# Kernel optimization log

Hardware: AMD Instinct MI355X
Metric: run time of the kernel (lower is better)

The kernel has to match this reference:

```python
import jax, jax.numpy as jnp
import numpy as np

WAY, NQ, C, H = 5, 150, 640, 10
TEMP, TEMP_ATTN = 0.2, 5.0


def _conv2d(x, w):
    return jax.lax.conv_general_dilated(x, w, (1, 1), ((0, 0), (0, 0)),
                                        dimension_numbers=('NCHW', 'OIHW', 'NCHW'))


def _conv3d(x, w, pad):
    return jax.lax.conv_general_dilated(x, w, (1, 1, 1), pad,
                                        dimension_numbers=('NCDHW', 'OIDHW', 'NCDHW'))


def _affine(x, g, b):
    # eval-mode BatchNorm folded to per-channel affine
    sh = (1, -1) + (1,) * (x.ndim - 2)
    return x * g.reshape(sh) + b.reshape(sh)


def _gnorm(x, axis, eps=1e-5):
    m = jnp.mean(x, axis=axis, keepdims=True)
    v = jnp.var(x, axis=axis, ddof=1, keepdims=True)  # torch.var is unbiased
    return (x - m) / jnp.sqrt(v + eps)


def _sep_conv4d(x, w2, g2, b2, w1, g1, b1, wp, gp, bp):
    # RENet SepConv4d: 3x3 conv over (Hs,Ws), relu, 3x3 conv over (Hq,Wq), 1x1 channel proj
    B, c, u, v, h, w = x.shape
    y = x.reshape(B, c, u, v, h * w)
    y = _conv3d(y, w2, ((1, 1), (1, 1), (0, 0)))  # kernel (3,3,1) over (u,v)
    y = jax.nn.relu(_affine(y, g2, b2))
    y = y.reshape(B, c, u * v, h, w)
    y = _conv3d(y, w1, ((0, 0), (1, 1), (1, 1)))  # kernel (1,3,3) over (h,w)
    y = _affine(y, g1, b1)
    y = _conv2d(y.reshape(B, c, u * v * h, w), wp)  # 1x1 projection to out channels
    y = _affine(y, gp, bp)
    return y.reshape(B, wp.shape[0], u, v, h, w)


def setup_inputs() -> dict:
    key = jax.random.key(0)
    ks = jax.random.split(key, 10)
    d = {}
    d['spt'] = jax.random.normal(ks[0], (1, WAY, C, H, H), jnp.float32)
    d['qry'] = jax.random.normal(ks[1], (NQ, C, H, H), jnp.float32)
    d['cca1x1_w'] = jax.random.normal(ks[2], (64, C, 1, 1), jnp.float32) * 0.05
    d['cca1x1_g'] = jnp.ones((64,), jnp.float32)
    d['cca1x1_b'] = jnp.zeros((64,), jnp.float32)
    # SepConv4d layer 0: 1 -> 16 channels
    d['s0_w2'] = jax.random.normal(ks[3], (1, 1, 3, 3, 1), jnp.float32) * 0.3
    d['s0_g2'] = jnp.ones((1,), jnp.float32); d['s0_b2'] = jnp.zeros((1,), jnp.float32)
    d['s0_w1'] = jax.random.normal(ks[4], (1, 1, 1, 3, 3), jnp.float32) * 0.3
    d['s0_g1'] = jnp.ones((1,), jnp.float32); d['s0_b1'] = jnp.zeros((1,), jnp.float32)
    d['s0_wp'] = jax.random.normal(ks[5], (16, 1, 1, 1), jnp.float32) * 0.3
    d['s0_gp'] = jnp.ones((16,), jnp.float32); d['s0_bp'] = jnp.zeros((16,), jnp.float32)
    # SepConv4d layer 1: 16 -> 1 channels
    d['s1_w2'] = jax.random.normal(ks[6], (16, 16, 3, 3, 1), jnp.float32) * 0.1
    d['s1_g2'] = jnp.ones((16,), jnp.float32); d['s1_b2'] = jnp.zeros((16,), jnp.float32)
    d['s1_w1'] = jax.random.normal(ks[7], (16, 16, 1, 3, 3), jnp.float32) * 0.1
    d['s1_g1'] = jnp.ones((16,), jnp.float32); d['s1_b1'] = jnp.zeros((16,), jnp.float32)
    d['s1_wp'] = jax.random.normal(ks[8], (1, 16, 1, 1), jnp.float32) * 0.3
    d['s1_gp'] = jnp.ones((1,), jnp.float32); d['s1_bp'] = jnp.zeros((1,), jnp.float32)
    return d


def reference(spt, qry, cca1x1_w, cca1x1_g, cca1x1_b,
              s0_w2, s0_g2, s0_b2, s0_w1, s0_g1, s0_b1, s0_wp, s0_gp, s0_bp,
              s1_w2, s1_g2, s1_b2, s1_w1, s1_g1, s1_b1, s1_wp, s1_gp, s1_bp):
    spt = spt[0]                                             # [way, C, H, W]
    spt = spt - jnp.mean(spt, axis=1, keepdims=True)         # normalize_feature
    qry = qry - jnp.mean(qry, axis=1, keepdims=True)

    def feat(x):
        y = jax.nn.relu(_affine(_conv2d(x, cca1x1_w), cca1x1_g, cca1x1_b))
        n = jnp.sqrt(jnp.sum(y * y, axis=1, keepdims=True))
        return y / jnp.maximum(n, 1e-8)                      # F.normalize(p=2, dim=1)

    s, q = feat(spt), feat(qry)                              # [way,64,H,W], [nq,64,H,W]
    corr = jnp.einsum('wcij,qckl->qwijkl', s, q)             # [nq,way,Hs,Ws,Hq,Wq]
    nq, way, Hs, Ws, Hq, Wq = corr.shape

    x = corr.reshape(nq * way, 1, Hs, Ws, Hq, Wq)
    x = _sep_conv4d(x, s0_w2, s0_g2, s0_b2, s0_w1, s0_g1, s0_b1, s0_wp, s0_gp, s0_bp)
    x = jax.nn.relu(x)
    x = _sep_conv4d(x, s1_w2, s1_g2, s1_b2, s1_w1, s1_g1, s1_b1, s1_wp, s1_gp, s1_bp)

    cs = _gnorm(x.reshape(nq, way, Hs * Ws, Hq, Wq), 2)
    cq = _gnorm(x.reshape(nq, way, Hs, Ws, Hq * Wq), 4)
    a_s = jax.nn.softmax(cs / TEMP_ATTN, axis=2).reshape(nq, way, Hs, Ws, Hq, Wq).sum(axis=(4, 5))
    a_q = jax.nn.softmax(cq / TEMP_ATTN, axis=4).reshape(nq, way, Hs, Ws, Hq, Wq).sum(axis=(2, 3))

    sp = (a_s[:, :, None] * spt[None]).mean(axis=(-1, -2))   # [nq,way,C]
    qp = (a_q[:, :, None] * qry[:, None]).mean(axis=(-1, -2))
    num = jnp.sum(sp * qp, axis=-1)
    den = jnp.maximum(jnp.linalg.norm(sp, axis=-1), 1e-8) * jnp.maximum(jnp.linalg.norm(qp, axis=-1), 1e-8)
    return (num / den) / TEMP                                # [nq, way]
```

## Files before the change

kernel.cpp:

```cpp
#include <hip/hip_runtime.h>
#include <cstdint>
#include <cstddef>

#define NQT   150
#define WAYT  5
#define CCH   640

typedef _Float16 f16;
typedef _Float16 f16x2 __attribute__((ext_vector_type(2)));
typedef _Float16 f16x4 __attribute__((ext_vector_type(4)));
typedef _Float16 f16x8 __attribute__((ext_vector_type(8)));
typedef float    f32x4 __attribute__((ext_vector_type(4)));

static __device__ __forceinline__ f16x2 pkrtz(float a, float b){
  return __builtin_bit_cast(f16x2, __builtin_amdgcn_cvt_pkrtz(a, b));
}

#define CP_A     0
#define CP_B     16
#define CP_G2    32
#define CP_B2    48
#define CP_W20   64
#define CP_W10   73
#define CP_SC    82
#define CP_T9    96
#define GS_STRIDE 1076

static __device__ __forceinline__ float stencil9(int k, int n, const float* __restrict__ w9){
  if (k >= 100 || n >= 100) return 0.f;
  const int a = n/10, b = n%10, a2 = k/10, b2 = k%10;
  const int dA = a2 - a + 1, dB = b2 - b + 1;
  if ((unsigned)dA > 2u || (unsigned)dB > 2u) return 0.f;
  return w9[dA*3 + dB];
}

__global__ __launch_bounds__(256) void k_prep_all(
    const float* __restrict__ W,
    const float* __restrict__ s0_w2, const float* __restrict__ s0_g2, const float* __restrict__ s0_b2,
    const float* __restrict__ s0_w1, const float* __restrict__ s0_g1, const float* __restrict__ s0_b1,
    const float* __restrict__ s0_wp, const float* __restrict__ s0_gp, const float* __restrict__ s0_bp,
    const float* __restrict__ s1_w2, const float* __restrict__ s1_g2, const float* __restrict__ s1_b2,
    const float* __restrict__ s1_w1, const float* __restrict__ s1_g1, const float* __restrict__ s1_b1,
    const float* __restrict__ s1_wp, const float* __restrict__ s1_gp, const float* __restrict__ s1_bp,
    float* __restrict__ cp, f16* __restrict__ Apack, f16* __restrict__ Wf2,
    f16* __restrict__ MuF, f16* __restrict__ MhF,
    f16* __restrict__ W65, float* __restrict__ wsum)
{
  const int b = blockIdx.x, t = threadIdx.x;
  if (b == 0){
    for (int e = t; e < 2560; e += 256){
      int p = e / 512, r = e % 512, l = r / 8, j = r % 8;
      int kb = l >> 4;
      int tap = 2*p + (kb >> 1);
      int cin = (kb & 1)*8 + j;
      int co = l & 15;
      float v = 0.f;
      if (tap <= 8){
        int du = tap / 3, dv = tap % 3;
        v = s1_w2[((co*16 + cin)*3 + du)*3 + dv];
      }
      Apack[e] = (f16)v;
    }
    const float gp1 = s1_gp[0];
    {
      int l = t >> 2, j = t & 3;
      int tap = l & 15, ci = ((l >> 4) << 2) + j;
      float v = 0.f;
      if (tap <= 8){
        for (int co = 0; co < 16; co++)
          v += gp1 * s1_wp[co] * s1_g1[co] * s1_w1[(co*16 + ci)*9 + tap];
      }
      Wf2[t] = (f16)v;
    }
    if (t < 144){
      int tap = t / 16, co = t % 16;
      float s = 0.f;
      for (int cin = 0; cin < 16; cin++){
        float wv = (float)(f16)s1_w2[((co*16 + cin)*3 + tap/3)*3 + tap%3];
        float rb = fmaxf((float)(f16)s0_bp[cin], 0.f);
        s += wv * rb;
      }
      cp[CP_T9 + t] = s;
    }
    if (t < 16){
      cp[CP_A + t]  = s0_gp[t] * s0_wp[t];
      cp[CP_B + t]  = s0_bp[t];
      cp[CP_G2 + t] = s1_g2[t];
      cp[CP_B2 + t] = s1_b2[t];
    }
    if (t < 9){ cp[CP_W20 + t] = s0_w2[t]; cp[CP_W10 + t] = s0_w1[t]; }
    if (t == 0){
      cp[CP_SC + 0] = s0_g2[0]; cp[CP_SC + 1] = s0_b2[0];
      cp[CP_SC + 2] = s0_g1[0]; cp[CP_SC + 3] = s0_b1[0];
      float kk = 0.f;
      for (int co = 0; co < 16; co++) kk += s1_wp[co] * s1_b1[co];
      cp[CP_SC + 4] = gp1 * kk + s1_bp[0];
    }
  } else if (b <= 14){
    const bool isMu = (b <= 7);
    f16* dst = isMu ? MuF : MhF;
    const float* w9 = isMu ? s0_w2 : s0_w1;
    const int base = (isMu ? (b-1) : (b-8)) * 2048;
    #pragma unroll
    for (int e2 = 0; e2 < 8; e2++){
      const int idx = base + e2*256 + t;
      const int j = idx & 7, l2 = (idx >> 3) & 63, ktnt = idx >> 9;
      const int kt = ktnt & 3, nt = ktnt >> 2;
      const int n = nt*16 + (l2 & 15);
      const int k = kt*32 + ((l2 >> 4) & 3)*8 + j;
      dst[idx] = (f16)stencil9(k, n, w9);
    }
  } else if (b <= 39){
    const int base = (b - 15) * 2048;
    #pragma unroll
    for (int e2 = 0; e2 < 8; e2++){
      const int idx = base + e2*256 + t;
      const int row = idx / 640, c = idx - row*640;
      float v = 0.f;
      if (row < 64) v = W[row*640 + c];
      else if (row == 64) v = 1.f;
      W65[idx] = (f16)v;
    }
  } else {
    const int o = t >> 2, qq = t & 3;
    float s = 0.f;
    for (int c = qq; c < 640; c += 4) s += W[o*640 + c];
    s += __shfl_xor(s, 1); s += __shfl_xor(s, 2);
    if (qq == 0) wsum[o] = s;
  }
}

__device__ __forceinline__ void feat_stage4(const float* __restrict__ x, int pixoff, int kt,
                                            f16* __restrict__ dst, int t){
  if (t < 224){
    const int cc = t / 7, qd = t % 7;
    float4 v4 = make_float4(0.f, 0.f, 0.f, 0.f);
    if (pixoff + qd*4 + 4 <= 100)
      v4 = *(const float4*)(x + (size_t)(kt*32 + cc)*100 + pixoff + qd*4);
    dst[(qd*4+0)*40 + cc] = (f16)v4.x;
    dst[(qd*4+1)*40 + cc] = (f16)v4.y;
    dst[(qd*4+2)*40 + cc] = (f16)v4.z;
    dst[(qd*4+3)*40 + cc] = (f16)v4.w;
  }
}

__global__ __launch_bounds__(256) void k_feat(
    const float* __restrict__ spt, const float* __restrict__ qry,
    const f16* __restrict__ W65, const float* __restrict__ wsum,
    const float* __restrict__ gg, const float* __restrict__ bb,
    f16* __restrict__ s16, f16* __restrict__ q16,
    float* __restrict__ sptm, float* __restrict__ qrym)
{
  __shared__ f16 Xs[2][32*40];
  __shared__ float Ys[32*85];
  __shared__ float sg[64], sb[64], sw[64];
  const int b = blockIdx.x;
  const int n = b >> 2, quarter = b & 3;
  const int pixbase = quarter * 28;
  const float* x; f16* out16; float* mout;
  if (n < 5){ x = spt + (size_t)n*64000; out16 = s16 + (size_t)n*7168; mout = sptm + n*100; }
  else { x = qry + (size_t)(n-5)*64000; out16 = q16 + (size_t)(n-5)*7168; mout = qrym + (size_t)(n-5)*100; }
  const int t = threadIdx.x, l = t & 63, wid = t >> 6;
  const int r16 = l & 15, kbq = (l >> 4) & 3;

  if (t < 40){
    const f16x8 z8 = {(f16)0,(f16)0,(f16)0,(f16)0,(f16)0,(f16)0,(f16)0,(f16)0};
    const int bu = t / 20, rr = (t % 20) / 5, o = t % 5;
    *(f16x8*)(Xs[bu] + (28 + rr)*40 + o*8) = z8;
  }
  if (t >= 64 && t < 128){ sg[t-64] = gg[t-64]; sb[t-64] = bb[t-64]; sw[t-64] = wsum[t-64]; }

  int mts[3], nts[3];
  #pragma unroll
  for (int s = 0; s < 3; s++){ const int mn = wid + s*4; mts[s] = mn >> 1; nts[s] = mn & 1; }
  f32x4 acc[3];
  #pragma unroll
  for (int s = 0; s < 3; s++) acc[s] = (f32x4){0.f,0.f,0.f,0.f};

  feat_stage4(x, pixbase, 0, Xs[0], t);
  __syncthreads();
  for (int kt = 0; kt < 20; kt++){
    if (kt < 19) feat_stage4(x, pixbase, kt+1, Xs[(kt+1)&1], t);
    const f16* xb = Xs[kt&1];
    #pragma unroll
    for (int s = 0; s < 3; s++){
      const int mn = wid + s*4;
      if (mn < 10){
        const f16x8 a8 = *(const f16x8*)(W65 + (size_t)(mts[s]*16 + r16)*640 + kt*32 + kbq*8);
        const f16x8 b8 = *(const f16x8*)(xb + (nts[s]*16 + r16)*40 + kbq*8);
        acc[s] = __builtin_amdgcn_mfma_f32_16x16x32_f16(a8, b8, acc[s], 0, 0, 0);
      }
    }
    __syncthreads();
  }
  #pragma unroll
  for (int s = 0; s < 3; s++){
    const int mn = wid + s*4;
    if (mn < 10){
      const int col = nts[s]*16 + r16, rb = mts[s]*16 + kbq*4;
      #pragma unroll
      for (int r = 0; r < 4; r++) Ys[col*85 + rb + r] = acc[s][r];
    }
  }
  __syncthreads();

  if (t < 224){
    const int pixl = t >> 3, oo = t & 7;
    const int pixg = pixbase + pixl;
    const bool ok = (pixg < 100);
    const float m = Ys[pixl*85 + 64] * (1.f/640.f);
    float yr[8]; float ssq = 0.f;
    #pragma unroll
    for (int j = 0; j < 8; j++){
      const int o = oo*8 + j;
      float yv = 0.f;
      if (ok) yv = fmaxf(sg[o]*(Ys[pixl*85 + o] - sw[o]*m) + sb[o], 0.f);
      yr[j] = yv; ssq += yv*yv;
    }
    ssq += __shfl_xor(ssq, 1); ssq += __shfl_xor(ssq, 2); ssq += __shfl_xor(ssq, 4);
    const float inv = ok ? (1.f / fmaxf(sqrtf(ssq), 1e-8f)) : 0.f;
    #pragma unroll
    for (int j2 = 0; j2 < 4; j2++){
      f16x2 hv = { (f16)(yr[2*j2]*inv), (f16)(yr[2*j2+1]*inv) };
      *(f16x2*)(out16 + (size_t)pixg*64 + oo*8 + 2*j2) = hv;
    }
    if (oo == 0 && ok) mout[pixg] = m;
  }
}

__global__ __launch_bounds__(256) void k_z(
    const f16* __restrict__ s16, const f16* __restrict__ q16,
    const float* __restrict__ cp, const f16* __restrict__ MuF, const f16* __restrict__ MhF,
    f16* __restrict__ z)
{
  __shared__ __align__(16) f16 smz[112*120 + 112*120 + 16];
  f16* cbT = smz;
  f16* tS  = smz + 112*120;
  const int pair = blockIdx.x;
  const int q = pair / WAYT, w = pair % WAYT;
  const int t = threadIdx.x, l = t & 63, wid = t >> 6;
  const int r16 = l & 15, kb = (l >> 4) & 3;

  {
    const f16x8 z8 = {(f16)0,(f16)0,(f16)0,(f16)0,(f16)0,(f16)0,(f16)0,(f16)0};
    if (t < 112){
      *(f16x8*)(cbT + t*120 + 112) = z8;
      *(f16x8*)(tS  + t*120 + 112) = z8;
    }
    if (t < 16) tS[112*120 + t] = (f16)0;
    if (t >= 240 && t < 248) tS[t - 240] = (f16)0;
  }

  const f16* sbase = s16 + (size_t)w * 7168;
  const f16* qbase = q16 + (size_t)q * 7168;

  for (int mn = wid; mn < 49; mn += 4){
    const int mt = mn / 7, nt = mn - (mn/7)*7;
    const f16x8 a0 = *(const f16x8*)(sbase + (mt*16 + r16)*64 + kb*8);
    const f16x8 a1 = *(const f16x8*)(sbase + (mt*16 + r16)*64 + 32 + kb*8);
    const f16x8 b0 = *(const f16x8*)(qbase + (nt*16 + r16)*64 + kb*8);
    const f16x8 b1 = *(const f16x8*)(qbase + (nt*16 + r16)*64 + 32 + kb*8);
    f32x4 acc = {0.f,0.f,0.f,0.f};
    acc = __builtin_amdgcn_mfma_f32_16x16x32_f16(a0, b0, acc, 0, 0, 0);
    acc = __builtin_amdgcn_mfma_f32_16x16x32_f16(a1, b1, acc, 0, 0, 0);
    union { f16x4 v4; f16x2 h2[2]; } hv;
    hv.h2[0] = pkrtz(acc[0], acc[1]);
    hv.h2[1] = pkrtz(acc[2], acc[3]);
    *(f16x4*)(cbT + (nt*16 + r16)*120 + mt*16 + kb*4) = hv.v4;
  }
  __syncthreads();

  const float g20 = cp[CP_SC+0], b20 = cp[CP_SC+1];
  for (int mn = wid; mn < 49; mn += 4){
    const int mt = mn / 7, nt = mn - (mn/7)*7;
    f32x4 acc = {0.f,0.f,0.f,0.f};
    #pragma unroll
    for (int kt = 0; kt < 4; kt++){
      const f16x8 a8 = *(const f16x8*)(cbT + (mt*16 + r16)*120 + kt*32 + kb*8);
      const f16x8 b8 = *(const f16x8*)(MuF + (size_t)(nt*4 + kt)*512 + l*8);
      acc = __builtin_amdgcn_mfma_f32_16x16x32_f16(a8, b8, acc, 0, 0, 0);
    }
    union { f16x4 v4; f16x2 h2[2]; } hv;
    hv.h2[0] = pkrtz(fmaxf(g20*acc[0] + b20, 0.f), fmaxf(g20*acc[1] + b20, 0.f));
    hv.h2[1] = pkrtz(fmaxf(g20*acc[2] + b20, 0.f), fmaxf(g20*acc[3] + b20, 0.f));
    *(f16x4*)(tS + (nt*16 + r16)*120 + mt*16 + kb*4) = hv.v4;
  }
  __syncthreads();

  const float g10 = cp[CP_SC+2], b10 = cp[CP_SC+3];
  for (int mn = wid; mn < 49; mn += 4){
    const int mt = mn / 7, nt = mn - (mn/7)*7;
    f32x4 acc = {0.f,0.f,0.f,0.f};
    #pragma unroll
    for (int kt = 0; kt < 4; kt++){
      const f16x8 a8 = *(const f16x8*)(tS + (mt*16 + r16)*120 + kt*32 + kb*8);
      const f16x8 b8 = *(const f16x8*)(MhF + (size_t)(nt*4 + kt)*512 + l*8);
      acc = __builtin_amdgcn_mfma_f32_16x16x32_f16(a8, b8, acc, 0, 0, 0);
    }
    const int hw = nt*16 + r16;
    if (hw < 100){
      #pragma unroll
      for (int r = 0; r < 4; r++){
        const int uv = mt*16 + kb*4 + r;
        if (uv < 100) z[(size_t)pair*10000 + uv*100 + hw] = (f16)(g10*acc[r] + b10);
      }
    }
  }
}

__global__ __launch_bounds__(256, 6) void k_l1(
    const f16* __restrict__ z, const float* __restrict__ cp,
    const f16* __restrict__ Apack, const f16* __restrict__ Wf2, f16* __restrict__ F)
{
  __shared__ f16 z3[3*1216];
  __shared__ f16 Gs[9*GS_STRIDE];
  const int u = blockIdx.x, pair = blockIdx.y;
  const int t = threadIdx.x, l = t & 63, wid = t >> 6;
  const int r16 = l & 15, kb = (l >> 4) & 3;
  const int khi = kb & 1, half = kb >> 1;

  for (int e = t; e < 1824; e += 256){
    const int du = e / 608, c2 = e - du*608;
    const int ur = u + du - 1;
    const int colb = c2*2;
    const int g = colb - 100;
    f16x2 v = {(f16)0, (f16)0};
    if (ur >= 0 && ur <= 9 && g >= 0 && g < 1000)
      v = *(const f16x2*)(z + (size_t)pair*10000 + ur*1000 + g);
    *(f16x2*)(z3 + du*1216 + colb) = v;
  }

  f16x2 Ac2[4], Bc2[4];
  {
    const float4 a4a = ((const float4*)(cp + CP_A))[khi*2];
    const float4 a4b = ((const float4*)(cp + CP_A))[khi*2+1];
    const float4 b4a = ((const float4*)(cp + CP_B))[khi*2];
    const float4 b4b = ((const float4*)(cp + CP_B))[khi*2+1];
    Ac2[0] = (f16x2){(f16)a4a.x,(f16)a4a.y}; Ac2[1] = (f16x2){(f16)a4a.z,(f16)a4a.w};
    Ac2[2] = (f16x2){(f16)a4b.x,(f16)a4b.y}; Ac2[3] = (f16x2){(f16)a4b.z,(f16)a4b.w};
    Bc2[0] = (f16x2){(f16)b4a.x,(f16)b4a.y}; Bc2[1] = (f16x2){(f16)b4a.z,(f16)b4a.w};
    Bc2[2] = (f16x2){(f16)b4b.x,(f16)b4b.y}; Bc2[3] = (f16x2){(f16)b4b.z,(f16)b4b.w};
  }
  f16x8 af[5];
  #pragma unroll
  for (int p = 0; p < 5; p++) af[p] = ((const f16x8*)Apack)[p*64 + l];
  const f16x4 wf = ((const f16x4*)Wf2)[l];

  float gv[4], bm[4], bv0[4], bv9[4];
  #pragma unroll
  for (int r = 0; r < 4; r++){
    const int co = kb*4 + r;
    gv[r] = cp[CP_G2 + co];
    const float b0 = cp[CP_B2 + co];
    float c0 = 0.f, cv0 = 0.f, cv9 = 0.f;
    #pragma unroll
    for (int du = 0; du < 3; du++){
      const int ur = u + du - 1;
      const float t0 = cp[CP_T9 + (du*3+0)*16 + co];
      const float t1 = cp[CP_T9 + (du*3+1)*16 + co];
      const float t2 = cp[CP_T9 + (du*3+2)*16 + co];
      if (ur < 0 || ur > 9) c0 += t0 + t1 + t2;
      else { cv0 += t0; cv9 += t2; }
    }
    bm[r]  = b0 - gv[r]*c0;
    bv0[r] = bm[r] - gv[r]*cv0;
    bv9[r] = bm[r] - gv[r]*cv9;
  }
  int zoffE[5];
  #pragma unroll
  for (int p = 0; p < 5; p++){
    const int tap = 2*p + half;
    const int du = (tap <= 8) ? tap/3 : 0;
    const int dv = (tap <= 8) ? tap%3 : 0;
    zoffE[p] = du*1216 + dv*100;
  }
  __syncthreads();

  const f16x2 zero2 = {(f16)0, (f16)0};
  #pragma unroll 1
  for (int i = 0; i < 16; i++){
    const int cbase = wid*256 + i*16;
    if (cbase >= 1008) break;
    const int c = cbase + r16;
    const int v = (c * 5243) >> 19;
    f32x4 acc = {0.f,0.f,0.f,0.f};
    #pragma unroll
    for (int p = 0; p < 5; p++){
      const f16 zv = z3[zoffE[p] + c];
      const f16x2 zz = {zv, zv};
      union { f16x8 v8; f16x2 h2[4]; } bu;
      #pragma unroll
      for (int j2 = 0; j2 < 4; j2++){
        f16x2 r2 = Ac2[j2] * zz + Bc2[j2];
        bu.h2[j2] = __builtin_elementwise_max(r2, zero2);
      }
      acc = __builtin_amdgcn_mfma_f32_16x16x32_f16(af[p], bu.v8, acc, 0, 0, 0);
    }
    const bool isv0 = (v == 0), isv9 = (v == 9);
    float rr[4];
    #pragma unroll
    for (int r = 0; r < 4; r++){
      const float bsel = isv0 ? bv0[r] : (isv9 ? bv9[r] : bm[r]);
      rr[r] = fmaxf(fmaf(gv[r], acc[r], bsel), 0.f);
    }
    union { f16x4 v4; f16x2 h2[2]; } t1u;
    t1u.h2[0] = pkrtz(rr[0], rr[1]);
    t1u.h2[1] = pkrtz(rr[2], rr[3]);
    f32x4 g = {0.f,0.f,0.f,0.f};
    g = __builtin_amdgcn_mfma_f32_16x16x16f16(wf, t1u.v4, g, 0, 0, 0);
    #pragma unroll
    for (int r = 0; r < 4; r++){
      const int tap = kb*4 + r;
      if (tap <= 8) Gs[tap*GS_STRIDE + 16 + c] = (f16)g[r];
    }
  }
  __syncthreads();

  const float Kc = cp[CP_SC+4];
  #pragma unroll 1
  for (int oo = 0; oo < 4; oo++){
    const int c = t + oo*256;
    if (c < 1000){
      const int hw = c - ((c * 5243) >> 19) * 100;
      const int h = (hw * 205) >> 11, w2 = hw - h*10;
      float o = Kc;
      #pragma unroll
      for (int dh = 0; dh < 3; dh++){
        #pragma unroll
        for (int dw = 0; dw < 3; dw++){
          const bool okg = ((unsigned)(h + dh - 1) <= 9u) && ((unsigned)(w2 + dw - 1) <= 9u);
          const float gvv = (float)Gs[(dh*3+dw)*GS_STRIDE + 16 + c + (dh-1)*10 + (dw-1)];
          o += okg ? gvv : 0.f;
        }
      }
      F[(size_t)pair*10000 + u*1000 + c] = (f16)o;
    }
  }
}

__global__ __launch_bounds__(256) void k_attn_a(const f16* __restrict__ F, float* __restrict__ asq)
{
  __shared__ float fb[100*101 + 4];
  __shared__ float isc[100], ccs[100], isr[100], ccr[100];
  const int pair = blockIdx.x;
  const int t = threadIdx.x;
  const float L2T = 1.4426950408889634f * 0.2f;

  for (int e = t; e < 10000; e += 256)
    fb[(e/100)*101 + (e%100)] = (float)F[(size_t)pair*10000 + e];
  __syncthreads();

  {
    const int line = t & 127;
    const bool isCol = t < 128;
    if (line < 100){
      const int base = isCol ? line : line*101;
      const int stride = isCol ? 101 : 1;
      float s = 0.f, ss = 0.f;
      for (int i = 0; i < 100; i++){ const float x = fb[base + i*stride]; s += x; ss += x*x; }
      const float m = s * 0.01f;
      const float var = (ss - 100.f*m*m) * (1.f/99.f);
      const float is2 = rsqrtf(var + 1e-5f) * L2T;
      float S = 0.f;
      for (int i = 0; i < 100; i++) S += exp2f((fb[base + i*stride] - m) * is2);
      const float cc = m*is2 + log2f(S);
      if (isCol){ isc[line] = is2; ccs[line] = cc; }
      else      { isr[line] = is2; ccr[line] = cc; }
    }
  }
  __syncthreads();
  {
    const int line = t & 127;
    if (line < 100){
      if (t < 128){
        float a = 0.f;
        for (int k = 0; k < 100; k++)
          a += exp2f(fb[line*101 + k] * isc[k] - ccs[k]);
        asq[(size_t)pair*256 + line] = a;
      } else {
        float a = 0.f;
        for (int k = 0; k < 100; k++)
          a += exp2f(fb[k*101 + line] * isr[k] - ccr[k]);
        asq[(size_t)pair*256 + 128 + line] = a;
      }
    } else {
      asq[(size_t)pair*256 + t] = 0.f;
    }
  }
}

__global__ __launch_bounds__(256) void k_spqp(
    const float* __restrict__ spt, const float* __restrict__ qry,
    const float* __restrict__ asq, float* __restrict__ P)
{
  const int b = blockIdx.x;
  const int t = threadIdx.x, l = t & 63, wid = t >> 6;
  const int r16 = l & 15, kb = (l >> 4) & 3;

  if (b < 50){
    const int w = b / 10, c0 = (b % 10) * 64;
    const int c = c0 + wid*16 + r16;
    f16x8 bf[4];
    #pragma unroll
    for (int kt = 0; kt < 4; kt++){
      const int kbase = kt*32 + kb*8;
      float v[8];
      #pragma unroll
      for (int j = 0; j < 8; j++){
        const int k = kbase + j;
        v[j] = (k < 100) ? spt[(size_t)w*64000 + (size_t)c*100 + k] : 0.f;
      }
      union { f16x8 v8; f16x2 h2[4]; } u;
      #pragma unroll
      for (int j2 = 0; j2 < 4; j2++) u.h2[j2] = pkrtz(v[2*j2], v[2*j2+1]);
      bf[kt] = u.v8;
    }
    #pragma unroll 1
    for (int mt = 0; mt < 10; mt++){
      const int qr = mt*16 + r16;
      f32x4 acc = {0.f,0.f,0.f,0.f};
      #pragma unroll
      for (int kt = 0; kt < 4; kt++){
        const int kbase = kt*32 + kb*8;
        float v[8];
        #pragma unroll
        for (int j = 0; j < 8; j++)
          v[j] = (qr < 150) ? asq[(size_t)(qr*5 + w)*256 + kbase + j] : 0.f;
        union { f16x8 v8; f16x2 h2[4]; } u;
        #pragma unroll
        for (int j2 = 0; j2 < 4; j2++) u.h2[j2] = pkrtz(v[2*j2], v[2*j2+1]);
        acc = __builtin_amdgcn_mfma_f32_16x16x32_f16(u.v8, bf[kt], acc, 0, 0, 0);
      }
      #pragma unroll
      for (int r = 0; r < 4; r++){
        const int q2 = mt*16 + kb*4 + r;
        if (q2 < 150) P[(size_t)(q2*5 + w)*1280 + c0 + wid*16 + (l & 15)] = acc[r];
      }
    }
  } else {
    const int idx = b - 50, q = idx >> 1, chalf = idx & 1;
    f16x8 af[4];
    #pragma unroll
    for (int kt = 0; kt < 4; kt++){
      const int kbase = kt*32 + kb*8;
      float v[8];
      #pragma unroll
      for (int j = 0; j < 8; j++)
        v[j] = (r16 < 5) ? asq[(size_t)(q*5 + r16)*256 + 128 + kbase + j] : 0.f;
      union { f16x8 v8; f16x2 h2[4]; } u;
      #pragma unroll
      for (int j2 = 0; j2 < 4; j2++) u.h2[j2] = pkrtz(v[2*j2], v[2*j2+1]);
      af[kt] = u.v8;
    }
    #pragma unroll 1
    for (int nt = chalf*20 + wid; nt < chalf*20 + 20; nt += 4){
      const int c = nt*16 + r16;
      f32x4 acc = {0.f,0.f,0.f,0.f};
      #pragma unroll
      for (int kt = 0; kt < 4; kt++){
        const int kbase = kt*32 + kb*8;
        float v[8];
        #pragma unroll
        for (int j = 0; j < 8; j++){
          const int k = kbase + j;
          v[j] = (k < 100) ? qry[(size_t)q*64000 + (size_t)c*100 + k] : 0.f;
        }
        union { f16x8 v8; f16x2 h2[4]; } u;
        #pragma unroll
        for (int j2 = 0; j2 < 4; j2++) u.h2[j2] = pkrtz(v[2*j2], v[2*j2+1]);
        acc = __builtin_amdgcn_mfma_f32_16x16x32_f16(af[kt], u.v8, acc, 0, 0, 0);
      }
      #pragma unroll
      for (int r = 0; r < 4; r++){
        const int w2 = kb*4 + r;
        if (w2 < 5) P[(size_t)(q*5 + w2)*1280 + 640 + nt*16 + (l & 15)] = acc[r];
      }
    }
  }
}

__global__ __launch_bounds__(256) void k_cos(
    const float* __restrict__ P, const float* __restrict__ asq,
    const float* __restrict__ sptm, const float* __restrict__ qrym,
    float* __restrict__ out)
{
  __shared__ float pred[4];
  __shared__ float MsMq[2];
  __shared__ float red[12];
  const int pair = blockIdx.x;
  const int q = pair / WAYT, w = pair % WAYT;
  const int t = threadIdx.x, wid = t >> 6;

  float pm = 0.f;
  if (t < 100) pm = asq[(size_t)pair*256 + t] * sptm[w*100 + t];
  else if (t >= 128 && t < 228) pm = asq[(size_t)pair*256 + t] * qrym[q*100 + (t - 128)];
  #pragma unroll
  for (int m = 1; m < 64; m <<= 1) pm += __shfl_xor(pm, m);
  if ((t & 63) == 0) pred[wid] = pm;
  __syncthreads();
  if (t == 0) MsMq[0] = pred[0] + pred[1];
  if (t == 1) MsMq[1] = pred[2] + pred[3];
  __syncthreads();
  const float Ms = MsMq[0], Mq = MsMq[1];

  float d0 = 0.f, d1 = 0.f, d2 = 0.f;
  for (int c = t; c < 640; c += 256){
    const float sp = P[(size_t)pair*1280 + c] - Ms;
    const float qp = P[(size_t)pair*1280 + 640 + c] - Mq;
    d0 += sp*qp; d1 += sp*sp; d2 += qp*qp;
  }
  #pragma unroll
  for (int m = 1; m < 64; m <<= 1){
    d0 += __shfl_xor(d0, m); d1 += __shfl_xor(d1, m); d2 += __shfl_xor(d2, m);
  }
  if ((t & 63) == 0){ red[wid*3+0] = d0; red[wid*3+1] = d1; red[wid*3+2] = d2; }
  __syncthreads();
  if (t == 0){
    float e0 = 0.f, e1 = 0.f, e2 = 0.f;
    #pragma unroll
    for (int k = 0; k < 4; k++){ e0 += red[k*3]; e1 += red[k*3+1]; e2 += red[k*3+2]; }
    const float den = fmaxf(sqrtf(e1), 1e-8f) * fmaxf(sqrtf(e2), 1e-8f);
    out[pair] = (e0 / den) * 5.0f;
  }
}

extern "C" void kernel_launch(void* const* d_in, const int* in_sizes, int n_in,
                              void* d_out, int out_size, void* d_ws, size_t ws_size,
                              hipStream_t stream)
{
  (void)in_sizes; (void)n_in; (void)out_size; (void)ws_size;
  const float* spt = (const float*)d_in[0];
  const float* qry = (const float*)d_in[1];
  const float* Wc  = (const float*)d_in[2];
  const float* gc  = (const float*)d_in[3];
  const float* bc  = (const float*)d_in[4];

  float* ws    = (float*)d_ws;
  float* cp    = ws;
  float* wsum  = ws + 256;
  float* sptm  = ws + 320;
  float* qrym  = ws + 820;
  f16*  Apack  = (f16*)(ws + 15872);
  f16*  Wf2    = (f16*)(ws + 17152);
  f16*  W65    = (f16*)(ws + 17280);
  f16*  MuF    = (f16*)(ws + 42880);
  f16*  MhF    = (f16*)(ws + 50048);
  f16*  s16    = (f16*)(ws + 57216);
  f16*  q16    = (f16*)(ws + 75136);
  f16*  z      = (f16*)(ws + 612736);
  f16*  F      = (f16*)(ws + 4362736);
  float* asq   = ws + 75136;
  float* P     = ws + 612736;

  k_prep_all<<<41, 256, 0, stream>>>(
      Wc,
      (const float*)d_in[5],  (const float*)d_in[6],  (const float*)d_in[7],
      (const float*)d_in[8],  (const float*)d_in[9],  (const float*)d_in[10],
      (const float*)d_in[11], (const float*)d_in[12], (const float*)d_in[13],
      (const float*)d_in[14], (const float*)d_in[15], (const float*)d_in[16],
      (const float*)d_in[17], (const float*)d_in[18], (const float*)d_in[19],
      (const float*)d_in[20], (const float*)d_in[21], (const float*)d_in[22],
      cp, Apack, Wf2, MuF, MhF, W65, wsum);
  k_feat<<<620, 256, 0, stream>>>(spt, qry, W65, wsum, gc, bc, s16, q16, sptm, qrym);
  k_z<<<NQT*WAYT, 256, 0, stream>>>(s16, q16, cp, MuF, MhF, z);
  {
    dim3 grid(10, NQT*WAYT);
    k_l1<<<grid, 256, 0, stream>>>(z, cp, Apack, Wf2, F);
  }
  k_attn_a<<<NQT*WAYT, 256, 0, stream>>>(F, asq);
  k_spqp<<<350, 256, 0, stream>>>(spt, qry, asq, P);
  k_cos<<<NQT*WAYT, 256, 0, stream>>>(P, asq, sptm, qrym, (float*)d_out);
}
```

Before: 252.5 us.

## Widen k_l1 to 512 threads, split tap 8 into 16x16x16 MFMA, prepack fp16 operands

k_l1 now launches 512 threads per block with eight waves. The padded ninth tap, previously handled by a fifth 16x16x32 MFMA, is now done with a smaller 16x16x16 MFMA using new prepacked Wf8 weights, and register arrays shrink. Separately, the support features are converted to fp16 in the prep kernel, and k_attn_a writes an fp16 copy of the attention sums. k_spqp then loads its MFMA operands as vectors instead of doing scalar fp32 loads and packing them. The workspace layout shifts to hold the new buffers, and the prep kernel gains 200 blocks.

```diff
diff --git a/kernel.cpp b/kernel.cpp
--- a/kernel.cpp
+++ b/kernel.cpp
@@ -35,16 +35,16 @@
 }
 
 __global__ __launch_bounds__(256) void k_prep_all(
-    const float* __restrict__ W,
+    const float* __restrict__ spt, const float* __restrict__ W,
     const float* __restrict__ s0_w2, const float* __restrict__ s0_g2, const float* __restrict__ s0_b2,
     const float* __restrict__ s0_w1, const float* __restrict__ s0_g1, const float* __restrict__ s0_b1,
     const float* __restrict__ s0_wp, const float* __restrict__ s0_gp, const float* __restrict__ s0_bp,
     const float* __restrict__ s1_w2, const float* __restrict__ s1_g2, const float* __restrict__ s1_b2,
     const float* __restrict__ s1_w1, const float* __restrict__ s1_g1, const float* __restrict__ s1_b1,
     const float* __restrict__ s1_wp, const float* __restrict__ s1_gp, const float* __restrict__ s1_bp,
-    float* __restrict__ cp, f16* __restrict__ Apack, f16* __restrict__ Wf2,
+    float* __restrict__ cp, f16* __restrict__ Apack, f16* __restrict__ Wf2, f16* __restrict__ Wf8,
     f16* __restrict__ MuF, f16* __restrict__ MhF,
-    f16* __restrict__ W65, float* __restrict__ wsum)
+    f16* __restrict__ W65, float* __restrict__ wsum, f16* __restrict__ spt16)
 {
   const int b = blockIdx.x, t = threadIdx.x;
   if (b == 0){
@@ -72,6 +72,11 @@
       }
       Wf2[t] = (f16)v;
     }
+    {
+      int l = t >> 2, j = t & 3;
+      int co = l & 15, cin = ((l >> 4) << 2) + j;
+      Wf8[t] = (f16)s1_w2[((co*16 + cin)*3 + 2)*3 + 2];
+    }
     if (t < 144){
       int tap = t / 16, co = t % 16;
       float s = 0.f;
@@ -121,12 +126,21 @@
       else if (row == 64) v = 1.f;
       W65[idx] = (f16)v;
     }
-  } else {
+  } else if (b == 40){
     const int o = t >> 2, qq = t & 3;
     float s = 0.f;
     for (int c = qq; c < 640; c += 4) s += W[o*640 + c];
     s += __shfl_xor(s, 1); s += __shfl_xor(s, 2);
     if (qq == 0) wsum[o] = s;
+  } else {
+    const int base = (b - 41) * 2048;
+    #pragma unroll
+    for (int e2 = 0; e2 < 8; e2++){
+      const int idx = base + e2*256 + t;
+      const int w = idx / 81920, r = idx % 81920;
+      const int c = r >> 7, k = r & 127;
+      spt16[idx] = (k < 100) ? (f16)spt[(size_t)w*64000 + c*100 + k] : (f16)0;
+    }
   }
 }
 
@@ -308,9 +322,10 @@
   }
 }
 
-__global__ __launch_bounds__(256, 6) void k_l1(
+__global__ __launch_bounds__(512, 8) void k_l1(
     const f16* __restrict__ z, const float* __restrict__ cp,
-    const f16* __restrict__ Apack, const f16* __restrict__ Wf2, f16* __restrict__ F)
+    const f16* __restrict__ Apack, const f16* __restrict__ Wf2, const f16* __restrict__ Wf8,
+    f16* __restrict__ F)
 {
   __shared__ f16 z3[3*1216];
   __shared__ f16 Gs[9*GS_STRIDE];
@@ -319,7 +334,7 @@
   const int r16 = l & 15, kb = (l >> 4) & 3;
   const int khi = kb & 1, half = kb >> 1;
 
-  for (int e = t; e < 1824; e += 256){
+  for (int e = t; e < 1824; e += 512){
     const int du = e / 608, c2 = e - du*608;
     const int ur = u + du - 1;
     const int colb = c2*2;
@@ -341,10 +356,18 @@
     Bc2[0] = (f16x2){(f16)b4a.x,(f16)b4a.y}; Bc2[1] = (f16x2){(f16)b4a.z,(f16)b4a.w};
     Bc2[2] = (f16x2){(f16)b4b.x,(f16)b4b.y}; Bc2[3] = (f16x2){(f16)b4b.z,(f16)b4b.w};
   }
-  f16x8 af[5];
-  #pragma unroll
-  for (int p = 0; p < 5; p++) af[p] = ((const f16x8*)Apack)[p*64 + l];
-  const f16x4 wf = ((const f16x4*)Wf2)[l];
+  f16x2 Ac8[2], Bc8[2];
+  {
+    const float4 a4 = ((const float4*)(cp + CP_A))[kb];
+    const float4 b4 = ((const float4*)(cp + CP_B))[kb];
+    Ac8[0] = (f16x2){(f16)a4.x,(f16)a4.y}; Ac8[1] = (f16x2){(f16)a4.z,(f16)a4.w};
+    Bc8[0] = (f16x2){(f16)b4.x,(f16)b4.y}; Bc8[1] = (f16x2){(f16)b4.z,(f16)b4.w};
+  }
+  f16x8 af[4];
+  #pragma unroll
+  for (int p = 0; p < 4; p++) af[p] = ((const f16x8*)Apack)[p*64 + l];
+  const f16x4 wf  = ((const f16x4*)Wf2)[l];
+  const f16x4 wf8 = ((const f16x4*)Wf8)[l];
 
   float gv[4], bm[4], bv0[4], bv9[4];
   #pragma unroll
@@ -366,26 +389,26 @@
     bv0[r] = bm[r] - gv[r]*cv0;
     bv9[r] = bm[r] - gv[r]*cv9;
   }
-  int zoffE[5];
-  #pragma unroll
-  for (int p = 0; p < 5; p++){
+  int zoffE[4];
+  #pragma unroll
+  for (int p = 0; p < 4; p++){
     const int tap = 2*p + half;
-    const int du = (tap <= 8) ? tap/3 : 0;
-    const int dv = (tap <= 8) ? tap%3 : 0;
+    const int du = tap/3, dv = tap%3;
     zoffE[p] = du*1216 + dv*100;
   }
+  const int zoff8 = 2*1216 + 2*100;
   __syncthreads();
 
   const f16x2 zero2 = {(f16)0, (f16)0};
   #pragma unroll 1
-  for (int i = 0; i < 16; i++){
-    const int cbase = wid*256 + i*16;
+  for (int i = 0; i < 8; i++){
+    const int cbase = (wid + i*8)*16;
     if (cbase >= 1008) break;
     const int c = cbase + r16;
     const int v = (c * 5243) >> 19;
     f32x4 acc = {0.f,0.f,0.f,0.f};
     #pragma unroll
-    for (int p = 0; p < 5; p++){
+    for (int p = 0; p < 4; p++){
       const f16 zv = z3[zoffE[p] + c];
       const f16x2 zz = {zv, zv};
       union { f16x8 v8; f16x2 h2[4]; } bu;
@@ -395,6 +418,14 @@
         bu.h2[j2] = __builtin_elementwise_max(r2, zero2);
       }
       acc = __builtin_amdgcn_mfma_f32_16x16x32_f16(af[p], bu.v8, acc, 0, 0, 0);
+    }
+    {
+      const f16 zv8 = z3[zoff8 + c];
+      const f16x2 z8 = {zv8, zv8};
+      union { f16x4 v4; f16x2 h2[2]; } b8u;
+      b8u.h2[0] = __builtin_elementwise_max(Ac8[0]*z8 + Bc8[0], zero2);
+      b8u.h2[1] = __builtin_elementwise_max(Ac8[1]*z8 + Bc8[1], zero2);
+      acc = __builtin_amdgcn_mfma_f32_16x16x16f16(wf8, b8u.v4, acc, 0, 0, 0);
     }
     const bool isv0 = (v == 0), isv9 = (v == 9);
     float rr[4];
@@ -418,8 +449,8 @@
 
   const float Kc = cp[CP_SC+4];
   #pragma unroll 1
-  for (int oo = 0; oo < 4; oo++){
-    const int c = t + oo*256;
+  for (int oo = 0; oo < 2; oo++){
+    const int c = t + oo*512;
     if (c < 1000){
       const int hw = c - ((c * 5243) >> 19) * 100;
       const int h = (hw * 205) >> 11, w2 = hw - h*10;
@@ -438,7 +469,8 @@
   }
 }
 
-__global__ __launch_bounds__(256) void k_attn_a(const f16* __restrict__ F, float* __restrict__ asq)
+__global__ __launch_bounds__(256) void k_attn_a(const f16* __restrict__ F,
+                                                float* __restrict__ asq, f16* __restrict__ asqh)
 {
   __shared__ float fb[100*101 + 4];
   __shared__ float isc[100], ccs[100], isr[100], ccr[100];
@@ -477,21 +509,24 @@
         for (int k = 0; k < 100; k++)
           a += exp2f(fb[line*101 + k] * isc[k] - ccs[k]);
         asq[(size_t)pair*256 + line] = a;
+        asqh[(size_t)pair*256 + line] = (f16)a;
       } else {
         float a = 0.f;
         for (int k = 0; k < 100; k++)
           a += exp2f(fb[k*101 + line] * isr[k] - ccr[k]);
         asq[(size_t)pair*256 + 128 + line] = a;
+        asqh[(size_t)pair*256 + 128 + line] = (f16)a;
       }
     } else {
       asq[(size_t)pair*256 + t] = 0.f;
+      asqh[(size_t)pair*256 + t] = (f16)0;
     }
   }
 }
 
 __global__ __launch_bounds__(256) void k_spqp(
-    const float* __restrict__ spt, const float* __restrict__ qry,
-    const float* __restrict__ asq, float* __restrict__ P)
+    const f16* __restrict__ spt16, const float* __restrict__ qry,
+    const f16* __restrict__ asqh, float* __restrict__ P)
 {
   const int b = blockIdx.x;
   const int t = threadIdx.x, l = t & 63, wid = t >> 6;
@@ -502,34 +537,16 @@
     const int c = c0 + wid*16 + r16;
     f16x8 bf[4];
     #pragma unroll
-    for (int kt = 0; kt < 4; kt++){
-      const int kbase = kt*32 + kb*8;
-      float v[8];
-      #pragma unroll
-      for (int j = 0; j < 8; j++){
-        const int k = kbase + j;
-        v[j] = (k < 100) ? spt[(size_t)w*64000 + (size_t)c*100 + k] : 0.f;
-      }
-      union { f16x8 v8; f16x2 h2[4]; } u;
-      #pragma unroll
-      for (int j2 = 0; j2 < 4; j2++) u.h2[j2] = pkrtz(v[2*j2], v[2*j2+1]);
-      bf[kt] = u.v8;
-    }
+    for (int kt = 0; kt < 4; kt++)
+      bf[kt] = *(const f16x8*)(spt16 + ((size_t)w*640 + c)*128 + kt*32 + kb*8);
     #pragma unroll 1
     for (int mt = 0; mt < 10; mt++){
       const int qr = mt*16 + r16;
       f32x4 acc = {0.f,0.f,0.f,0.f};
       #pragma unroll
       for (int kt = 0; kt < 4; kt++){
-        const int kbase = kt*32 + kb*8;
-        float v[8];
-        #pragma unroll
-        for (int j = 0; j < 8; j++)
-          v[j] = (qr < 150) ? asq[(size_t)(qr*5 + w)*256 + kbase + j] : 0.f;
-        union { f16x8 v8; f16x2 h2[4]; } u;
-        #pragma unroll
-        for (int j2 = 0; j2 < 4; j2++) u.h2[j2] = pkrtz(v[2*j2], v[2*j2+1]);
-        acc = __builtin_amdgcn_mfma_f32_16x16x32_f16(u.v8, bf[kt], acc, 0, 0, 0);
+        const f16x8 au = *(const f16x8*)(asqh + (size_t)(qr*5 + w)*256 + kt*32 + kb*8);
+        acc = __builtin_amdgcn_mfma_f32_16x16x32_f16(au, bf[kt], acc, 0, 0, 0);
       }
       #pragma unroll
       for (int r = 0; r < 4; r++){
@@ -539,19 +556,10 @@
     }
   } else {
     const int idx = b - 50, q = idx >> 1, chalf = idx & 1;
-    f16x8 af[4];
-    #pragma unroll
-    for (int kt = 0; kt < 4; kt++){
-      const int kbase = kt*32 + kb*8;
-      float v[8];
-      #pragma unroll
-      for (int j = 0; j < 8; j++)
-        v[j] = (r16 < 5) ? asq[(size_t)(q*5 + r16)*256 + 128 + kbase + j] : 0.f;
-      union { f16x8 v8; f16x2 h2[4]; } u;
-      #pragma unroll
-      for (int j2 = 0; j2 < 4; j2++) u.h2[j2] = pkrtz(v[2*j2], v[2*j2+1]);
-      af[kt] = u.v8;
-    }
+    f16x8 af4[4];
+    #pragma unroll
+    for (int kt = 0; kt < 4; kt++)
+      af4[kt] = *(const f16x8*)(asqh + (size_t)(q*5 + r16)*256 + 128 + kt*32 + kb*8);
     #pragma unroll 1
     for (int nt = chalf*20 + wid; nt < chalf*20 + 20; nt += 4){
       const int c = nt*16 + r16;
@@ -565,10 +573,10 @@
           const int k = kbase + j;
           v[j] = (k < 100) ? qry[(size_t)q*64000 + (size_t)c*100 + k] : 0.f;
         }
-        union { f16x8 v8; f16x2 h2[4]; } u;
+        union { f16x8 v8; f16x2 h2[4]; } uu;
         #pragma unroll
-        for (int j2 = 0; j2 < 4; j2++) u.h2[j2] = pkrtz(v[2*j2], v[2*j2+1]);
-        acc = __builtin_amdgcn_mfma_f32_16x16x32_f16(af[kt], u.v8, acc, 0, 0, 0);
+        for (int j2 = 0; j2 < 4; j2++) uu.h2[j2] = pkrtz(v[2*j2], v[2*j2+1]);
+        acc = __builtin_amdgcn_mfma_f32_16x16x32_f16(af4[kt], uu.v8, acc, 0, 0, 0);
       }
       #pragma unroll
       for (int r = 0; r < 4; r++){
@@ -642,32 +650,35 @@
   float* qrym  = ws + 820;
   f16*  Apack  = (f16*)(ws + 15872);
   f16*  Wf2    = (f16*)(ws + 17152);
-  f16*  W65    = (f16*)(ws + 17280);
-  f16*  MuF    = (f16*)(ws + 42880);
-  f16*  MhF    = (f16*)(ws + 50048);
-  f16*  s16    = (f16*)(ws + 57216);
-  f16*  q16    = (f16*)(ws + 75136);
-  f16*  z      = (f16*)(ws + 612736);
-  f16*  F      = (f16*)(ws + 4362736);
-  float* asq   = ws + 75136;
-  float* P     = ws + 612736;
-
-  k_prep_all<<<41, 256, 0, stream>>>(
-      Wc,
+  f16*  Wf8    = (f16*)(ws + 17280);
+  f16*  W65    = (f16*)(ws + 17408);
+  f16*  MuF    = (f16*)(ws + 43008);
+  f16*  MhF    = (f16*)(ws + 50176);
+  f16*  s16    = (f16*)(ws + 57344);
+  f16*  q16    = (f16*)(ws + 75264);
+  f16*  z      = (f16*)(ws + 612864);
+  f16*  F      = (f16*)(ws + 4362864);
+  f16*  spt16  = (f16*)(ws + 8112864);
+  float* asq   = ws + 75264;
+  f16*  asqh   = (f16*)(ws + 75264 + 192000);
+  float* P     = ws + 612864;
+
+  k_prep_all<<<241, 256, 0, stream>>>(
+      spt, Wc,
       (const float*)d_in[5],  (const float*)d_in[6],  (const float*)d_in[7],
       (const float*)d_in[8],  (const float*)d_in[9],  (const float*)d_in[10],
       (const float*)d_in[11], (const float*)d_in[12], (const float*)d_in[13],
       (const float*)d_in[14], (const float*)d_in[15], (const float*)d_in[16],
       (const float*)d_in[17], (const float*)d_in[18], (const float*)d_in[19],
       (const float*)d_in[20], (const float*)d_in[21], (const float*)d_in[22],
-      cp, Apack, Wf2, MuF, MhF, W65, wsum);
+      cp, Apack, Wf2, Wf8, MuF, MhF, W65, wsum, spt16);
   k_feat<<<620, 256, 0, stream>>>(spt, qry, W65, wsum, gc, bc, s16, q16, sptm, qrym);
   k_z<<<NQT*WAYT, 256, 0, stream>>>(s16, q16, cp, MuF, MhF, z);
   {
     dim3 grid(10, NQT*WAYT);
-    k_l1<<<grid, 256, 0, stream>>>(z, cp, Apack, Wf2, F);
-  }
-  k_attn_a<<<NQT*WAYT, 256, 0, stream>>>(F, asq);
-  k_spqp<<<350, 256, 0, stream>>>(spt, qry, asq, P);
+    k_l1<<<grid, 512, 0, stream>>>(z, cp, Apack, Wf2, Wf8, F);
+  }
+  k_attn_a<<<NQT*WAYT, 256, 0, stream>>>(F, asq, asqh);
+  k_spqp<<<350, 256, 0, stream>>>(spt16, qry, asqh, P);
   k_cos<<<NQT*WAYT, 256, 0, stream>>>(P, asq, sptm, qrym, (float*)d_out);
 }
```

New measurement: 315.4 us. 1.25x slower.
